# Optimization experiments

Hardware: AMD Instinct MI355X
Metric: run time of the kernel (lower is better)

Reference implementation:

```python
import jax, jax.numpy as jnp
import numpy as np

HIDDEN = 2048
NUM_HEADS = 32
HEAD_DIM = 64
NUM_KV = 8
GROUP = NUM_HEADS // NUM_KV
SCALE = HEAD_DIM ** -0.5
ROPE_BASE = 10000.0


def apply_rope(t):
    # t: [B, H, S, D]; standard half-split rotary embedding
    S, D = t.shape[-2], t.shape[-1]
    inv_freq = 1.0 / (ROPE_BASE ** (jnp.arange(0, D, 2, dtype=jnp.float32) / D))  # [D/2]
    ang = jnp.arange(S, dtype=jnp.float32)[:, None] * inv_freq[None, :]           # [S, D/2]
    cos, sin = jnp.cos(ang), jnp.sin(ang)
    x1, x2 = t[..., : D // 2], t[..., D // 2 :]
    return jnp.concatenate([x1 * cos - x2 * sin, x2 * cos + x1 * sin], axis=-1)


def setup_inputs() -> dict:
    key = jax.random.key(0)
    ks = jax.random.split(key, 10)
    B, S = 2, 2048
    s_in = HIDDEN ** -0.5
    s_o = (NUM_HEADS * HEAD_DIM) ** -0.5
    return {
        "x": jax.random.normal(ks[0], (B, S, HIDDEN), jnp.float32),
        "Wq": jax.random.normal(ks[1], (NUM_HEADS * HEAD_DIM, HIDDEN), jnp.float32) * s_in,
        "bq": jnp.zeros((NUM_HEADS * HEAD_DIM,), jnp.float32),
        "Wk": jax.random.normal(ks[2], (NUM_KV * HEAD_DIM, HIDDEN), jnp.float32) * s_in,
        "bk": jnp.zeros((NUM_KV * HEAD_DIM,), jnp.float32),
        "Wv": jax.random.normal(ks[3], (NUM_KV * HEAD_DIM, HIDDEN), jnp.float32) * s_in,
        "bv": jnp.zeros((NUM_KV * HEAD_DIM,), jnp.float32),
        "Wo": jax.random.normal(ks[4], (HIDDEN, NUM_HEADS * HEAD_DIM), jnp.float32) * s_o,
        "bo": jnp.zeros((HIDDEN,), jnp.float32),
        "key_weights": jax.random.normal(ks[5], (NUM_HEADS,), jnp.float32),
    }


def reference(x, Wq, bq, Wk, bk, Wv, bv, Wo, bo, key_weights):
    B, S, _ = x.shape
    q = (x @ Wq.T + bq).reshape(B, S, NUM_HEADS, HEAD_DIM).transpose(0, 2, 1, 3)
    k = (x @ Wk.T + bk).reshape(B, S, NUM_KV, HEAD_DIM).transpose(0, 2, 1, 3)
    v = (x @ Wv.T + bv).reshape(B, S, NUM_KV, HEAD_DIM).transpose(0, 2, 1, 3)
    q = apply_rope(q)
    k = apply_rope(k)
    # group queries per KV head: [B, kv, g, S, D]
    qg = q.reshape(B, NUM_KV, GROUP, S, HEAD_DIM)
    scores = jnp.einsum("bkgsd,bktd->bkgst", qg, k) * SCALE
    scores = scores * key_weights.reshape(1, NUM_KV, GROUP, 1, 1)
    causal = jnp.tril(jnp.ones((S, S), bool))
    scores = jnp.where(causal, scores, -jnp.inf)
    a = jax.nn.softmax(scores, axis=-1)
    o = jnp.einsum("bkgst,bktd->bkgsd", a, v)  # [B, kv, g, S, D]
    o = o.reshape(B, NUM_HEADS, S, HEAD_DIM).transpose(0, 2, 1, 3).reshape(B, S, NUM_HEADS * HEAD_DIM)
    return o @ Wo.T + bo
```

## Files before the change

kernel.cpp:

```cpp
#include <hip/hip_runtime.h>
#include <stdint.h>

#define S_LEN 2048
#define HID   2048
#define NH    32
#define NKV   8
#define HD    64
#define BATCH 2
#define NROWS (BATCH * S_LEN)
#define QKVN  (NH*HD + 2*NKV*HD)

typedef unsigned short u16;
typedef __bf16 bf16_t;
typedef bf16_t bf16x8 __attribute__((ext_vector_type(8)));
typedef float  f32x4  __attribute__((ext_vector_type(4)));
typedef float  f32x16 __attribute__((ext_vector_type(16)));
typedef u16    u16x8  __attribute__((ext_vector_type(8)));

#define LOG2E 1.4426950408889634f

__device__ __forceinline__ u16 f2bf(float f) {
    union { float f; uint32_t u; } v; v.f = f;
    uint32_t u = v.u;
    return (u16)((u + 0x7fffu + ((u >> 16) & 1u)) >> 16);
}

__device__ __forceinline__ unsigned cvtpk(float a, float b) {
    unsigned r;
    asm("v_cvt_pk_bf16_f32 %0, %1, %2" : "=v"(r) : "v"(a), "v"(b));
    return r;
}

__device__ __forceinline__ void plswap(unsigned &a, unsigned &b) {
    asm volatile("v_permlane32_swap_b32 %0, %1" : "+v"(a), "+v"(b));
}

__device__ __forceinline__ void llds16(const void* g, void* l) {
    __builtin_amdgcn_global_load_lds(
        (const __attribute__((address_space(1))) void*)g,
        (__attribute__((address_space(3))) void*)l,
        16, 0, 0);
}

__global__ void cvt_all(const float* __restrict__ x, const float* __restrict__ wq,
                        const float* __restrict__ wk, const float* __restrict__ wv,
                        const float* __restrict__ wo,
                        u16* __restrict__ xb, u16* __restrict__ wqkvb, u16* __restrict__ wob) {
    int e = blockIdx.x * 256 + threadIdx.x;
    const float* s; u16* d; int o;
    if (e < 1048576)      { s = x;  d = xb;                 o = e; }
    else if (e < 1572864) { s = wq; d = wqkvb;              o = e - 1048576; }
    else if (e < 1703936) { s = wk; d = wqkvb + 2048*2048;  o = e - 1572864; }
    else if (e < 1835008) { s = wv; d = wqkvb + 2560*2048;  o = e - 1703936; }
    else                  { s = wo; d = wob;                o = e - 1835008; }
    const float4* sp = (const float4*)s;
    float4 a = sp[2*(size_t)o], b = sp[2*(size_t)o + 1];
    u16x8 r;
    r[0]=f2bf(a.x); r[1]=f2bf(a.y); r[2]=f2bf(a.z); r[3]=f2bf(a.w);
    r[4]=f2bf(b.x); r[5]=f2bf(b.y); r[6]=f2bf(b.z); r[7]=f2bf(b.w);
    *(u16x8*)(d + 8*(size_t)o) = r;
}

__global__ void build_bqkv(const float* __restrict__ bq, const float* __restrict__ bk,
                           const float* __restrict__ bv, float* __restrict__ bqkv) {
    int i = blockIdx.x * 256 + threadIdx.x;
    if (i >= QKVN) return;
    bqkv[i] = (i < 2048) ? bq[i] : (i < 2560 ? bk[i - 2048] : bv[i - 2560]);
}

__global__ void rope_table(float* __restrict__ tab) {
    int idx = blockIdx.x * 256 + threadIdx.x;
    if (idx >= S_LEN * 32) return;
    int i = idx & 31, s = idx >> 5;
    float invf = exp2f(-(float)i * (13.287712379549449f / 32.0f));
    float ang = (float)s * invf;
    float sn, cs;
    sincosf(ang, &sn, &cs);
    tab[idx] = cs;
    tab[S_LEN*32 + idx] = sn;
}

__global__ __launch_bounds__(256) void gemm_qkv(
    const u16* __restrict__ A, const u16* __restrict__ Bw,
    const float* __restrict__ bias, const float* __restrict__ rtab,
    const float* __restrict__ kw,
    u16* __restrict__ qpk, u16* __restrict__ kpk, u16* __restrict__ vlin)
{
    const int M = NROWS, N = QKVN, K = HID;
    const int nbm = M >> 7, nbn = N >> 7;
    const int nwg = nbm * nbn;
    int wg = blockIdx.x;
    wg = (wg & 7) * (nwg >> 3) + (wg >> 3);
    const int bm = wg % nbm, bn = wg / nbm;
    const int brow = bm << 7, bcol = bn << 7;

    __shared__ u16 sA[128 * 32];
    __shared__ u16 sB[128 * 32];

    const int t = threadIdx.x;
    const int lane = t & 63, wid = t >> 6;
    const int wr = wid >> 1, wc = wid & 1;
    const int lr = lane & 15, lhi = lane >> 4;

    f32x4 acc[4][4] = {};

    for (int k0 = 0; k0 < K; k0 += 32) {
        __syncthreads();
        #pragma unroll
        for (int i = 0; i < 2; ++i) {
            const unsigned off = ((unsigned)t << 4) + ((unsigned)i << 12);
            const unsigned row = off >> 6;
            const unsigned ce  = (off & 63) >> 1;
            llds16(A  + (size_t)(brow + row) * K + (k0 + ce), sA + (off >> 1));
            llds16(Bw + (size_t)(bcol + row) * K + (k0 + ce), sB + (off >> 1));
        }
        __syncthreads();
        bf16x8 af[4], bfv[4];
        #pragma unroll
        for (int m = 0; m < 4; ++m)
            af[m] = *(const bf16x8*)(sA + ((wr*64 + m*16 + lr) * 32 + lhi*8));
        #pragma unroll
        for (int n = 0; n < 4; ++n)
            bfv[n] = *(const bf16x8*)(sB + ((wc*64 + n*16 + lr) * 32 + lhi*8));
        #pragma unroll
        for (int m = 0; m < 4; ++m)
            #pragma unroll
            for (int n = 0; n < 4; ++n)
                acc[m][n] = __builtin_amdgcn_mfma_f32_16x16x32_bf16(af[m], bfv[n], acc[m][n], 0, 0, 0);
    }

    const int c64 = bcol + wc*64;
    const int hb  = c64 >> 6;
    const int rowb = brow + wr*64;

    if (hb < 40) {
        const bool isQ = hb < 32;
        const float sc = isQ ? (0.125f * LOG2E * kw[hb]) : 1.0f;
        u16* dst = isQ ? qpk : kpk;
        const int nheads = isQ ? 32 : 8;
        const int hloc = isQ ? hb : (hb - 32);
        #pragma unroll
        for (int m = 0; m < 4; ++m) {
            #pragma unroll
            for (int n = 0; n < 2; ++n) {
                const int i = n*16 + lr;
                const float b1 = bias[c64 + i];
                const float b2 = bias[c64 + i + 32];
                #pragma unroll
                for (int j = 0; j < 4; ++j) {
                    const int row = rowb + m*16 + lhi*4 + j;
                    const int s = row & (S_LEN - 1);
                    const int bb = row >> 11;
                    const float x1 = acc[m][n][j] + b1;
                    const float x2 = acc[m][n+2][j] + b2;
                    const float cs = rtab[s*32 + i];
                    const float sn = rtab[S_LEN*32 + s*32 + i];
                    const size_t base = ((size_t)(bb*nheads + hloc)) * (S_LEN*64) + (size_t)s*64;
                    dst[base + i]      = f2bf((x1*cs - x2*sn) * sc);
                    dst[base + i + 32] = f2bf((x2*cs + x1*sn) * sc);
                }
            }
        }
    } else {
        #pragma unroll
        for (int m = 0; m < 4; ++m) {
            #pragma unroll
            for (int n = 0; n < 4; ++n) {
                const int col = c64 + n*16 + lr;
                const float bv = bias[col];
                #pragma unroll
                for (int j = 0; j < 4; ++j) {
                    const int row = rowb + m*16 + lhi*4 + j;
                    vlin[(size_t)row * 512 + (col - 2560)] = f2bf(acc[m][n][j] + bv);
                }
            }
        }
    }
}

__global__ __launch_bounds__(256) void gemm_bt(
    const u16* __restrict__ A, const u16* __restrict__ Bw,
    const float* __restrict__ bias, float* __restrict__ C,
    int M, int N, int K)
{
    const int nbm = M >> 7, nbn = N >> 7;
    const int nwg = nbm * nbn;
    int wg = blockIdx.x;
    wg = (wg & 7) * (nwg >> 3) + (wg >> 3);
    const int bm = wg % nbm, bn = wg / nbm;
    const int brow = bm << 7, bcol = bn << 7;

    __shared__ u16 sA[128 * 32];
    __shared__ u16 sB[128 * 32];

    const int t = threadIdx.x;
    const int lane = t & 63, wid = t >> 6;
    const int wr = wid >> 1, wc = wid & 1;
    const int lr = lane & 15, lhi = lane >> 4;

    f32x4 acc[4][4] = {};

    for (int k0 = 0; k0 < K; k0 += 32) {
        __syncthreads();
        #pragma unroll
        for (int i = 0; i < 2; ++i) {
            const unsigned off = ((unsigned)t << 4) + ((unsigned)i << 12);
            const unsigned row = off >> 6;
            const unsigned ce  = (off & 63) >> 1;
            llds16(A  + (size_t)(brow + row) * K + (k0 + ce), sA + (off >> 1));
            llds16(Bw + (size_t)(bcol + row) * K + (k0 + ce), sB + (off >> 1));
        }
        __syncthreads();
        bf16x8 af[4], bfv[4];
        #pragma unroll
        for (int m = 0; m < 4; ++m)
            af[m] = *(const bf16x8*)(sA + ((wr*64 + m*16 + lr) * 32 + lhi*8));
        #pragma unroll
        for (int n = 0; n < 4; ++n)
            bfv[n] = *(const bf16x8*)(sB + ((wc*64 + n*16 + lr) * 32 + lhi*8));
        #pragma unroll
        for (int m = 0; m < 4; ++m)
            #pragma unroll
            for (int n = 0; n < 4; ++n)
                acc[m][n] = __builtin_amdgcn_mfma_f32_16x16x32_bf16(af[m], bfv[n], acc[m][n], 0, 0, 0);
    }

    #pragma unroll
    for (int m = 0; m < 4; ++m) {
        #pragma unroll
        for (int n = 0; n < 4; ++n) {
            const int col = bcol + wc*64 + n*16 + lr;
            const float bv = bias[col];
            #pragma unroll
            for (int j = 0; j < 4; ++j) {
                const int row = brow + wr*64 + m*16 + lhi*4 + j;
                C[(size_t)row * N + col] = acc[m][n][j] + bv;
            }
        }
    }
}

__global__ void pack_vt(const u16* __restrict__ vlin, u16* __restrict__ vtb) {
    __shared__ u16 tile[64][67];
    const int st = blockIdx.x;
    const int bk = blockIdx.y;
    const int t = threadIdx.x;
    const int b = bk >> 3, kvh = bk & 7;
    const int r = t >> 2, cg = (t & 3) << 4;
    const u16* src = vlin + ((size_t)(b*S_LEN + st*64 + r)) * 512 + kvh*64 + cg;
    #pragma unroll
    for (int j = 0; j < 16; ++j) tile[r][cg + j] = src[j];
    __syncthreads();
    const int d = t >> 2, sg = (t & 3) << 4;
    u16* dst = vtb + ((size_t)(bk*64 + d)) * S_LEN + st*64 + sg;
    #pragma unroll
    for (int j = 0; j < 16; ++j) dst[j] = tile[sg + j][d];
}

__global__ __launch_bounds__(512, 4) void attn_fwd(
    const u16* __restrict__ Q,
    const u16* __restrict__ Kk,
    const u16* __restrict__ Vt,
    u16* __restrict__ O)
{
    __shared__ u16 sK[2][64 * 64];
    __shared__ u16 sV[2][64 * 64];

    const int t = threadIdx.x;
    const int lane = t & 63, wid = t >> 6;
    const int hi = lane >> 5, lq = lane & 31;
    const int bid = blockIdx.x;
    const int qb = (bid < 256) ? (7 - (bid >> 6)) : ((bid >> 6) - 4);
    const int bh = bid & 63;
    const int b = bh >> 5, h = bh & 31;
    const int kvh = h >> 2;

    const u16* Kp = Kk + ((size_t)(b*NKV + kvh)) * (S_LEN * 64);
    const u16* Vp = Vt + ((size_t)(b*NKV + kvh)) * (64 * S_LEN);

    const int q0w = qb*256 + wid*32;
    const int qg  = q0w + lq;

    const u16* Qrow = Q + (((size_t)bh) * S_LEN + qg) * 64 + 8*hi;
    bf16x8 qf[4];
    #pragma unroll
    for (int kd = 0; kd < 4; ++kd)
        qf[kd] = *(const bf16x8*)(Qrow + 16*kd);

    f32x16 accO0 = {}, accO1 = {};
    float m_run = 0.f, l_run = 0.f;

    const int ntB = 4*qb + 4;
    const int tmax_w = (q0w + 31) >> 6;

    {
        const unsigned row = t >> 3, cb = (t & 7) << 4;
        const unsigned scb = cb ^ ((row & 7) << 4);
        llds16(Kp + (size_t)row * 64 + (scb >> 1), &sK[0][0] + t*8);
        llds16(Vp + (size_t)row * S_LEN + (scb >> 1), &sV[0][0] + t*8);
    }
    asm volatile("s_waitcnt vmcnt(0)" ::: "memory");
    __syncthreads();

    for (int tt = 0; tt < ntB; ++tt) {
        const int buf = tt & 1;
        const int kv0 = tt * 64;
        if (tt + 1 < ntB) {
            const int kvn = kv0 + 64;
            const unsigned row = t >> 3, cb = (t & 7) << 4;
            const unsigned scb = cb ^ ((row & 7) << 4);
            llds16(Kp + (size_t)(kvn + row) * 64 + (scb >> 1), &sK[buf^1][0] + t*8);
            llds16(Vp + (size_t)row * S_LEN + kvn + (scb >> 1), &sV[buf^1][0] + t*8);
        }
        if (tt <= tmax_w) {
            const float nm = -m_run;
            f32x16 s0, s1;
            #pragma unroll
            for (int r = 0; r < 16; ++r) { s0[r] = nm; s1[r] = nm; }
            #pragma unroll
            for (int kd = 0; kd < 4; ++kd) {
                const unsigned bc = ((unsigned)(32*kd + 16*hi)) ^ ((lq & 7) << 4);
                bf16x8 k0 = *(const bf16x8*)((const char*)&sK[buf][0] + lq*128 + bc);
                bf16x8 k1 = *(const bf16x8*)((const char*)&sK[buf][0] + (32 + lq)*128 + bc);
                s0 = __builtin_amdgcn_mfma_f32_32x32x16_bf16(k0, qf[kd], s0, 0, 0, 0);
                s1 = __builtin_amdgcn_mfma_f32_32x32x16_bf16(k1, qf[kd], s1, 0, 0, 0);
            }
            if (kv0 + 63 > q0w) {
                #pragma unroll
                for (int r = 0; r < 16; ++r) {
                    const int kvg = kv0 + (r & 3) + 8*(r >> 2) + 4*hi;
                    if (kvg > qg)      s0[r] = -INFINITY;
                    if (kvg + 32 > qg) s1[r] = -INFINITY;
                }
            }
            float mx[8];
            #pragma unroll
            for (int r = 0; r < 8; ++r)
                mx[r] = fmaxf(fmaxf(s0[r], s0[r+8]), fmaxf(s1[r], s1[r+8]));
            float tm = fmaxf(fmaxf(fmaxf(mx[0], mx[1]), fmaxf(mx[2], mx[3])),
                             fmaxf(fmaxf(mx[4], mx[5]), fmaxf(mx[6], mx[7])));
            tm = fmaxf(tm, __shfl_xor(tm, 32));
            if (!__all(tm <= 8.0f)) {
                const float dd = fmaxf(tm, 0.f);
                const float al = __builtin_amdgcn_exp2f(-dd);
                m_run += dd;
                l_run *= al;
                #pragma unroll
                for (int r = 0; r < 16; ++r) { accO0[r] *= al; accO1[r] *= al; }
                #pragma unroll
                for (int r = 0; r < 16; ++r) { s0[r] -= dd; s1[r] -= dd; }
            }
            #pragma unroll
            for (int r = 0; r < 16; ++r) {
                s0[r] = __builtin_amdgcn_exp2f(s0[r]);
                s1[r] = __builtin_amdgcn_exp2f(s1[r]);
            }
            float sm[8];
            #pragma unroll
            for (int r = 0; r < 8; ++r)
                sm[r] = (s0[r] + s0[r+8]) + (s1[r] + s1[r+8]);
            float rs = ((sm[0]+sm[1]) + (sm[2]+sm[3])) + ((sm[4]+sm[5]) + (sm[6]+sm[7]));
            rs += __shfl_xor(rs, 32);
            l_run += rs;

            #pragma unroll
            for (int ks = 0; ks < 4; ++ks) {
                const f32x16& e = (ks & 2) ? s1 : s0;
                const int rb = (ks & 1) * 8;
                unsigned x0 = cvtpk(e[rb + 0], e[rb + 1]);
                unsigned x1 = cvtpk(e[rb + 2], e[rb + 3]);
                unsigned y0 = cvtpk(e[rb + 4], e[rb + 5]);
                unsigned y1 = cvtpk(e[rb + 6], e[rb + 7]);
                plswap(x0, y0);
                plswap(x1, y1);
                union { unsigned u[4]; bf16x8 v; } pb;
                pb.u[0] = x0; pb.u[1] = x1; pb.u[2] = y0; pb.u[3] = y1;
                const unsigned bc = ((unsigned)(32*ks + 16*hi)) ^ ((lq & 7) << 4);
                bf16x8 v0 = *(const bf16x8*)((const char*)&sV[buf][0] + lq*128 + bc);
                bf16x8 v1 = *(const bf16x8*)((const char*)&sV[buf][0] + (32 + lq)*128 + bc);
                accO0 = __builtin_amdgcn_mfma_f32_32x32x16_bf16(v0, pb.v, accO0, 0, 0, 0);
                accO1 = __builtin_amdgcn_mfma_f32_32x32x16_bf16(v1, pb.v, accO1, 0, 0, 0);
            }
        }
        asm volatile("s_waitcnt vmcnt(0)" ::: "memory");
        __syncthreads();
    }

    const float inv = 1.0f / l_run;
    u16* orow = O + (((size_t)(b * S_LEN) + q0w + lq)) * (NH*HD) + h*64;
    #pragma unroll
    for (int g = 0; g < 4; ++g) {
        uint2 w0, w1;
        w0.x = cvtpk(accO0[4*g + 0] * inv, accO0[4*g + 1] * inv);
        w0.y = cvtpk(accO0[4*g + 2] * inv, accO0[4*g + 3] * inv);
        *(uint2*)(orow + 8*g + 4*hi) = w0;
        w1.x = cvtpk(accO1[4*g + 0] * inv, accO1[4*g + 1] * inv);
        w1.y = cvtpk(accO1[4*g + 2] * inv, accO1[4*g + 3] * inv);
        *(uint2*)(orow + 32 + 8*g + 4*hi) = w1;
    }
}

extern "C" void kernel_launch(void* const* d_in, const int* in_sizes, int n_in,
                              void* d_out, int out_size, void* d_ws, size_t ws_size,
                              hipStream_t stream) {
    const float* x  = (const float*)d_in[0];
    const float* Wq = (const float*)d_in[1];
    const float* bq = (const float*)d_in[2];
    const float* Wk = (const float*)d_in[3];
    const float* bk = (const float*)d_in[4];
    const float* Wv = (const float*)d_in[5];
    const float* bv = (const float*)d_in[6];
    const float* Wo = (const float*)d_in[7];
    const float* bo = (const float*)d_in[8];
    const float* kw = (const float*)d_in[9];

    uint8_t* ws = (uint8_t*)d_ws;
    u16*   xb    = (u16*)(ws);
    u16*   wqkvb = (u16*)(ws + 16777216);
    u16*   wob   = (u16*)(ws + 29360128);
    u16*   qpk   = (u16*)(ws + 37748736);
    u16*   kpk   = (u16*)(ws + 54525952);
    u16*   vlin  = (u16*)(ws + 58720256);
    u16*   vtb   = (u16*)(ws + 62914560);
    u16*   ob    = (u16*)(ws + 67108864);
    float* bqkv  = (float*)(ws + 83886080);
    float* rtab  = (float*)(ws + 83898368);

    cvt_all<<<9216, 256, 0, stream>>>(x, Wq, Wk, Wv, Wo, xb, wqkvb, wob);
    build_bqkv<<<12, 256, 0, stream>>>(bq, bk, bv, bqkv);
    rope_table<<<256, 256, 0, stream>>>(rtab);

    gemm_qkv<<<768, 256, 0, stream>>>(xb, wqkvb, bqkv, rtab, kw, qpk, kpk, vlin);

    pack_vt<<<dim3(32, 16), 256, 0, stream>>>(vlin, vtb);

    attn_fwd<<<dim3(512), dim3(512), 0, stream>>>(qpk, kpk, vtb, ob);

    gemm_bt<<<512, 256, 0, stream>>>(ob, wob, bo, (float*)d_out, NROWS, HID, HID);

    (void)in_sizes; (void)n_in; (void)out_size; (void)ws_size;
}
```

Baseline: 223.0 us.

## Triple-buffer LDS tiles with one barrier per iteration in GEMMs and attention

```diff
diff --git a/kernel.cpp b/kernel.cpp
--- a/kernel.cpp
+++ b/kernel.cpp
@@ -41,6 +41,12 @@
         (__attribute__((address_space(3))) void*)l,
         16, 0, 0);
 }
+
+#define CBAR(N) do { \
+    asm volatile("s_waitcnt vmcnt(" #N ")" ::: "memory"); \
+    __builtin_amdgcn_s_barrier(); \
+    __builtin_amdgcn_sched_barrier(0); \
+} while (0)
 
 __global__ void cvt_all(const float* __restrict__ x, const float* __restrict__ wq,
                         const float* __restrict__ wk, const float* __restrict__ wv,
@@ -94,27 +100,36 @@
     const int bm = wg % nbm, bn = wg / nbm;
     const int brow = bm << 7, bcol = bn << 7;
 
-    __shared__ u16 sA[128 * 32];
-    __shared__ u16 sB[128 * 32];
+    __shared__ u16 sbuf[3][8192];
 
     const int t = threadIdx.x;
     const int lane = t & 63, wid = t >> 6;
     const int wr = wid >> 1, wc = wid & 1;
     const int lr = lane & 15, lhi = lane >> 4;
 
-    f32x4 acc[4][4] = {};
-
-    for (int k0 = 0; k0 < K; k0 += 32) {
-        __syncthreads();
+    auto stage = [&](int kt, int bi) {
+        const int k0 = kt << 5;
         #pragma unroll
         for (int i = 0; i < 2; ++i) {
             const unsigned off = ((unsigned)t << 4) + ((unsigned)i << 12);
             const unsigned row = off >> 6;
             const unsigned ce  = (off & 63) >> 1;
-            llds16(A  + (size_t)(brow + row) * K + (k0 + ce), sA + (off >> 1));
-            llds16(Bw + (size_t)(bcol + row) * K + (k0 + ce), sB + (off >> 1));
-        }
-        __syncthreads();
+            llds16(A  + (size_t)(brow + row) * K + (k0 + ce), &sbuf[bi][0]    + (off >> 1));
+            llds16(Bw + (size_t)(bcol + row) * K + (k0 + ce), &sbuf[bi][4096] + (off >> 1));
+        }
+    };
+
+    f32x4 acc[4][4] = {};
+    const int nk = K >> 5;
+
+    stage(0, 0);
+    stage(1, 1);
+    int cur = 0, st2 = 2;
+    for (int kt = 0; kt < nk; ++kt) {
+        if (kt < nk - 1) CBAR(4); else CBAR(0);
+        if (kt + 2 < nk) stage(kt + 2, st2);
+        const u16* sA = &sbuf[cur][0];
+        const u16* sB = &sbuf[cur][4096];
         bf16x8 af[4], bfv[4];
         #pragma unroll
         for (int m = 0; m < 4; ++m)
@@ -127,6 +142,8 @@
             #pragma unroll
             for (int n = 0; n < 4; ++n)
                 acc[m][n] = __builtin_amdgcn_mfma_f32_16x16x32_bf16(af[m], bfv[n], acc[m][n], 0, 0, 0);
+        cur = (cur == 2) ? 0 : cur + 1;
+        st2 = (st2 == 2) ? 0 : st2 + 1;
     }
 
     const int c64 = bcol + wc*64;
@@ -190,27 +207,36 @@
     const int bm = wg % nbm, bn = wg / nbm;
     const int brow = bm << 7, bcol = bn << 7;
 
-    __shared__ u16 sA[128 * 32];
-    __shared__ u16 sB[128 * 32];
+    __shared__ u16 sbuf[3][8192];
 
     const int t = threadIdx.x;
     const int lane = t & 63, wid = t >> 6;
     const int wr = wid >> 1, wc = wid & 1;
     const int lr = lane & 15, lhi = lane >> 4;
 
-    f32x4 acc[4][4] = {};
-
-    for (int k0 = 0; k0 < K; k0 += 32) {
-        __syncthreads();
+    auto stage = [&](int kt, int bi) {
+        const int k0 = kt << 5;
         #pragma unroll
         for (int i = 0; i < 2; ++i) {
             const unsigned off = ((unsigned)t << 4) + ((unsigned)i << 12);
             const unsigned row = off >> 6;
             const unsigned ce  = (off & 63) >> 1;
-            llds16(A  + (size_t)(brow + row) * K + (k0 + ce), sA + (off >> 1));
-            llds16(Bw + (size_t)(bcol + row) * K + (k0 + ce), sB + (off >> 1));
-        }
-        __syncthreads();
+            llds16(A  + (size_t)(brow + row) * K + (k0 + ce), &sbuf[bi][0]    + (off >> 1));
+            llds16(Bw + (size_t)(bcol + row) * K + (k0 + ce), &sbuf[bi][4096] + (off >> 1));
+        }
+    };
+
+    f32x4 acc[4][4] = {};
+    const int nk = K >> 5;
+
+    stage(0, 0);
+    stage(1, 1);
+    int cur = 0, st2 = 2;
+    for (int kt = 0; kt < nk; ++kt) {
+        if (kt < nk - 1) CBAR(4); else CBAR(0);
+        if (kt + 2 < nk) stage(kt + 2, st2);
+        const u16* sA = &sbuf[cur][0];
+        const u16* sB = &sbuf[cur][4096];
         bf16x8 af[4], bfv[4];
         #pragma unroll
         for (int m = 0; m < 4; ++m)
@@ -223,6 +249,8 @@
             #pragma unroll
             for (int n = 0; n < 4; ++n)
                 acc[m][n] = __builtin_amdgcn_mfma_f32_16x16x32_bf16(af[m], bfv[n], acc[m][n], 0, 0, 0);
+        cur = (cur == 2) ? 0 : cur + 1;
+        st2 = (st2 == 2) ? 0 : st2 + 1;
     }
 
     #pragma unroll
@@ -263,8 +291,8 @@
     const u16* __restrict__ Vt,
     u16* __restrict__ O)
 {
-    __shared__ u16 sK[2][64 * 64];
-    __shared__ u16 sV[2][64 * 64];
+    __shared__ u16 sK[3][64 * 64];
+    __shared__ u16 sV[3][64 * 64];
 
     const int t = threadIdx.x;
     const int lane = t & 63, wid = t >> 6;
@@ -293,26 +321,23 @@
     const int ntB = 4*qb + 4;
     const int tmax_w = (q0w + 31) >> 6;
 
-    {
+    auto stageKV = [&](int kt, int bi) {
+        const int kv = kt << 6;
         const unsigned row = t >> 3, cb = (t & 7) << 4;
         const unsigned scb = cb ^ ((row & 7) << 4);
-        llds16(Kp + (size_t)row * 64 + (scb >> 1), &sK[0][0] + t*8);
-        llds16(Vp + (size_t)row * S_LEN + (scb >> 1), &sV[0][0] + t*8);
-    }
-    asm volatile("s_waitcnt vmcnt(0)" ::: "memory");
-    __syncthreads();
+        llds16(Kp + (size_t)(kv + row) * 64 + (scb >> 1), &sK[bi][0] + t*8);
+        llds16(Vp + (size_t)row * S_LEN + kv + (scb >> 1), &sV[bi][0] + t*8);
+    };
+
+    stageKV(0, 0);
+    stageKV(1, 1);
+    int cur = 0, st2 = 2;
 
     for (int tt = 0; tt < ntB; ++tt) {
-        const int buf = tt & 1;
-        const int kv0 = tt * 64;
-        if (tt + 1 < ntB) {
-            const int kvn = kv0 + 64;
-            const unsigned row = t >> 3, cb = (t & 7) << 4;
-            const unsigned scb = cb ^ ((row & 7) << 4);
-            llds16(Kp + (size_t)(kvn + row) * 64 + (scb >> 1), &sK[buf^1][0] + t*8);
-            llds16(Vp + (size_t)row * S_LEN + kvn + (scb >> 1), &sV[buf^1][0] + t*8);
-        }
+        if (tt < ntB - 1) CBAR(2); else CBAR(0);
+        if (tt + 2 < ntB) stageKV(tt + 2, st2);
         if (tt <= tmax_w) {
+            const int kv0 = tt * 64;
             const float nm = -m_run;
             f32x16 s0, s1;
             #pragma unroll
@@ -320,8 +345,8 @@
             #pragma unroll
             for (int kd = 0; kd < 4; ++kd) {
                 const unsigned bc = ((unsigned)(32*kd + 16*hi)) ^ ((lq & 7) << 4);
-                bf16x8 k0 = *(const bf16x8*)((const char*)&sK[buf][0] + lq*128 + bc);
-                bf16x8 k1 = *(const bf16x8*)((const char*)&sK[buf][0] + (32 + lq)*128 + bc);
+                bf16x8 k0 = *(const bf16x8*)((const char*)&sK[cur][0] + lq*128 + bc);
+                bf16x8 k1 = *(const bf16x8*)((const char*)&sK[cur][0] + (32 + lq)*128 + bc);
                 s0 = __builtin_amdgcn_mfma_f32_32x32x16_bf16(k0, qf[kd], s0, 0, 0, 0);
                 s1 = __builtin_amdgcn_mfma_f32_32x32x16_bf16(k1, qf[kd], s1, 0, 0, 0);
             }
@@ -376,14 +401,14 @@
                 union { unsigned u[4]; bf16x8 v; } pb;
                 pb.u[0] = x0; pb.u[1] = x1; pb.u[2] = y0; pb.u[3] = y1;
                 const unsigned bc = ((unsigned)(32*ks + 16*hi)) ^ ((lq & 7) << 4);
-                bf16x8 v0 = *(const bf16x8*)((const char*)&sV[buf][0] + lq*128 + bc);
-                bf16x8 v1 = *(const bf16x8*)((const char*)&sV[buf][0] + (32 + lq)*128 + bc);
+                bf16x8 v0 = *(const bf16x8*)((const char*)&sV[cur][0] + lq*128 + bc);
+                bf16x8 v1 = *(const bf16x8*)((const char*)&sV[cur][0] + (32 + lq)*128 + bc);
                 accO0 = __builtin_amdgcn_mfma_f32_32x32x16_bf16(v0, pb.v, accO0, 0, 0, 0);
                 accO1 = __builtin_amdgcn_mfma_f32_32x32x16_bf16(v1, pb.v, accO1, 0, 0, 0);
             }
         }
-        asm volatile("s_waitcnt vmcnt(0)" ::: "memory");
-        __syncthreads();
+        cur = (cur == 2) ? 0 : cur + 1;
+        st2 = (st2 == 2) ? 0 : st2 + 1;
     }
 
     const float inv = 1.0f / l_run;
```

Measured after the change: 194.1 us. 12.9% less time.
